# Optimization experiments

Measured on AMD Instinct MI355X. Metric: run time of the kernel, lower is better.

The kernel has to match this reference:

```python
import jax, jax.numpy as jnp
import numpy as np

K = 4                                   # children per internal node (complete K-ary tree)
L = 7                                   # number of tree levels
N = (K**L - 1) // (K - 1)               # 5461 nodes, BFS order, root = node 0
IN_DIM = 512
MEM_DIM = 512
_STARTS = [(K**l - 1) // (K - 1) for l in range(L + 1)]  # node-index range of each level


def _make_children():
    ch = np.full((N, K), -1, dtype=np.int32)
    for n in range(N):
        base = n * K + 1
        if base + K <= N:                # internal node; leaves keep -1 padding
            ch[n] = np.arange(base, base + K, dtype=np.int32)
    return jnp.asarray(ch)


def setup_inputs() -> dict:
    key = jax.random.key(0)
    ks = jax.random.split(key, 40)
    it = iter(range(1, 40))

    def lin(fin, fout):
        s = 1.0 / np.sqrt(fin)           # torch nn.Linear default init
        W = jax.random.uniform(ks[next(it)], (fin, fout), jnp.float32, -s, s)
        b = jax.random.uniform(ks[next(it)], (fout,), jnp.float32, -s, s)
        return W, b

    inp = {
        "x": jax.random.normal(ks[0], (N, IN_DIM), jnp.float32),
        "children": _make_children(),
    }
    for mod in ("vis", "lang"):
        inp[f"W_ioux_{mod}"], inp[f"b_ioux_{mod}"] = lin(IN_DIM, 3 * MEM_DIM)
        inp[f"W_iouh_{mod}"], inp[f"b_iouh_{mod}"] = lin(MEM_DIM, 3 * MEM_DIM)
        inp[f"W_fx_{mod}"], inp[f"b_fx_{mod}"] = lin(IN_DIM, MEM_DIM)
        inp[f"W_fh_{mod}"], inp[f"b_fh_{mod}"] = lin(MEM_DIM, MEM_DIM)
    inp["W_type"], inp["b_type"] = lin(IN_DIM, 2)
    return inp


def _gates(iou_x, fx_n, W_iouh, b_iouh, W_fh, b_fh, child_c, child_h, h_sum):
    # iou_x: [n,3m] precomputed ioux(x); fx_n: [n,m]; child_*: [n,K,m]; h_sum: [n,m]
    iou = iou_x + h_sum @ W_iouh + b_iouh
    i, o, u = jnp.split(iou, 3, axis=-1)
    f = jax.nn.sigmoid(child_h @ W_fh + b_fh + fx_n[:, None, :])   # [n,K,m]
    c = jax.nn.sigmoid(i) * jnp.tanh(u) + (f * child_c).sum(axis=1)
    h = jax.nn.sigmoid(o) * jnp.tanh(c)
    return c, h


def reference(x, children,
              W_ioux_vis, b_ioux_vis, W_iouh_vis, b_iouh_vis,
              W_fx_vis, b_fx_vis, W_fh_vis, b_fh_vis,
              W_ioux_lang, b_ioux_lang, W_iouh_lang, b_iouh_lang,
              W_fx_lang, b_fx_lang, W_fh_lang, b_fh_lang,
              W_type, b_type):
    dt = x.dtype
    # input-side projections for every node at once (batched GEMMs)
    ioux_v = x @ W_ioux_vis + b_ioux_vis
    fx_v = x @ W_fx_vis + b_fx_vis
    ioux_l = x @ W_ioux_lang + b_ioux_lang
    fx_l = x @ W_fx_lang + b_fx_lang
    # eval-mode greedy type selection: one-hot argmax of type_query logits
    sel_lang = jnp.argmax(x @ W_type + b_type, axis=-1) == 0       # [N] True -> lang branch

    c_all = jnp.zeros((N, MEM_DIM), dt)
    h_all = jnp.zeros((N, MEM_DIM), dt)

    for l in range(L - 1, -1, -1):       # bottom-up over tree levels (static loop)
        s, e = _STARTS[l], _STARTS[l + 1]
        ch = children[s:e]               # [n,K]
        m = (ch >= 0)[..., None].astype(dt)
        idx = jnp.where(ch >= 0, ch, 0)
        child_c = c_all[idx] * m         # leaves: all-zero child states (matches original)
        child_h = h_all[idx] * m
        h_sum = child_h.sum(axis=1)
        c_v, h_v = _gates(ioux_v[s:e], fx_v[s:e], W_iouh_vis, b_iouh_vis,
                          W_fh_vis, b_fh_vis, child_c, child_h, h_sum)
        c_l, h_l = _gates(ioux_l[s:e], fx_l[s:e], W_iouh_lang, b_iouh_lang,
                          W_fh_lang, b_fh_lang, child_c, child_h, h_sum)
        lang = sel_lang[s:e][:, None]
        c_all = c_all.at[s:e].set(jnp.where(lang, c_l, c_v))
        h_all = h_all.at[s:e].set(jnp.where(lang, h_l, h_v))
    return h_all                         # up-state h of every node; root at row 0
```

## Files before the change

### kernel.cpp

```cpp
#include <hip/hip_runtime.h>
#include <cstdint>

constexpr int N_NODES = 5461;
constexpr int N_INTERIOR = 1365;

using f16x8 = __attribute__((ext_vector_type(8))) _Float16;
using f32x4 = __attribute__((ext_vector_type(4))) float;

typedef const __attribute__((address_space(1))) unsigned int* gas_p;
typedef __attribute__((address_space(3))) unsigned int* las_p;

__device__ __forceinline__ float sigm(float v) { return 1.0f / (1.0f + __expf(-v)); }

__constant__ int d_STARTS[8] = {0, 1, 5, 21, 85, 341, 1365, 5461};

struct GP {
    const _Float16* Ah[2]; const _Float16* Al[2];
    const _Float16* BhL[2]; const _Float16* BlL[2];
    const _Float16* BhV[2]; const _Float16* BlV[2];
    const float* biasL[2]; const float* biasV[2];
    float* Y[2];
    const int* permA[2];
    const int* cntPtr;
    int cntScale[2];
    int M[2]; int Nout[2]; int yT0;
};

__global__ __launch_bounds__(512, 4)
void gemm_pair(GP g)
{
    const int set = (blockIdx.y < (unsigned)g.yT0) ? 0 : 1;
    const int bn = (set ? (blockIdx.y - g.yT0) : blockIdx.y) * 128;
    const int M = g.M[set];
    const int Nout = g.Nout[set];
    const int nL = g.cntPtr[0] * g.cntScale[set];
    const int nTl = (nL + 127) >> 7;
    const int t = blockIdx.x;
    int rowBase, rowEnd;
    const _Float16 *Bh, *Bl;
    const float* bias;
    if (t < nTl) {
        rowBase = t << 7; rowEnd = nL;
        Bh = g.BhL[set]; Bl = g.BlL[set]; bias = g.biasL[set];
    } else {
        rowBase = nL + ((t - nTl) << 7); rowEnd = M;
        Bh = g.BhV[set]; Bl = g.BlV[set]; bias = g.biasV[set];
    }
    if (rowBase >= rowEnd) return;

    __shared__ _Float16 AsH[2][128 * 32];
    __shared__ _Float16 AsL[2][128 * 32];
    __shared__ _Float16 BsH[2][128 * 32];
    __shared__ _Float16 BsL[2][128 * 32];

    const int tid = threadIdx.x;
    const int wid = tid >> 6;
    const int lane = tid & 63;
    const int wm = (wid >> 2) * 64;
    const int wn = (wid & 3) * 32;
    const int lrow = lane >> 2;
    const int kofs = (lane & 3) * 8;

    int u0 = rowBase + wid * 16 + lrow; if (u0 > rowEnd - 1) u0 = rowEnd - 1;
    const int* permA = g.permA[set];
    const int a0 = permA ? permA[u0] : u0;
    const _Float16* gAh = g.Ah[set] + (size_t)a0 * 512 + kofs;
    const _Float16* gAl = g.Al[set] + (size_t)a0 * 512 + kofs;
    const _Float16* gBh = Bh + (size_t)(bn + wid * 16 + lrow) * 512 + kofs;
    const _Float16* gBl = Bl + (size_t)(bn + wid * 16 + lrow) * 512 + kofs;

    f32x4 acc0[4][2] = {};
    f32x4 acc1[4][2] = {};

    auto stage = [&](int k0, int b) {
        __builtin_amdgcn_global_load_lds((gas_p)(const void*)(gAh + k0), (las_p)(void*)(&AsH[b][wid * 512]), 16, 0, 0);
        __builtin_amdgcn_global_load_lds((gas_p)(const void*)(gAl + k0), (las_p)(void*)(&AsL[b][wid * 512]), 16, 0, 0);
        __builtin_amdgcn_global_load_lds((gas_p)(const void*)(gBh + k0), (las_p)(void*)(&BsH[b][wid * 512]), 16, 0, 0);
        __builtin_amdgcn_global_load_lds((gas_p)(const void*)(gBl + k0), (las_p)(void*)(&BsL[b][wid * 512]), 16, 0, 0);
    };

    const int rsel = lane & 15;
    const int kg = lane >> 4;

    stage(0, 0);
    __syncthreads();
#pragma unroll 1
    for (int step = 0; step < 16; ++step) {
        const int cur = step & 1;
        if (step < 15) stage((step + 1) * 32, cur ^ 1);
        const f16x8* AH = (const f16x8*)AsH[cur];
        const f16x8* AL = (const f16x8*)AsL[cur];
        const f16x8* BH = (const f16x8*)BsH[cur];
        const f16x8* BL = (const f16x8*)BsL[cur];
        f16x8 bh[2], bl[2];
#pragma unroll
        for (int j = 0; j < 2; ++j) {
            bh[j] = BH[(wn + j * 16 + rsel) * 4 + kg];
            bl[j] = BL[(wn + j * 16 + rsel) * 4 + kg];
        }
#pragma unroll
        for (int i = 0; i < 4; ++i) {
            f16x8 ah = AH[(wm + i * 16 + rsel) * 4 + kg];
            f16x8 al = AL[(wm + i * 16 + rsel) * 4 + kg];
#pragma unroll
            for (int j = 0; j < 2; ++j) {
                acc0[i][j] = __builtin_amdgcn_mfma_f32_16x16x32_f16(ah, bh[j], acc0[i][j], 0, 0, 0);
                acc1[i][j] = __builtin_amdgcn_mfma_f32_16x16x32_f16(ah, bl[j], acc1[i][j], 0, 0, 0);
                acc1[i][j] = __builtin_amdgcn_mfma_f32_16x16x32_f16(al, bh[j], acc1[i][j], 0, 0, 0);
            }
        }
        __syncthreads();
    }

    float* Y = g.Y[set];
#pragma unroll
    for (int i = 0; i < 4; ++i) {
        int row0 = rowBase + wm + i * 16 + kg * 4;
#pragma unroll
        for (int j = 0; j < 2; ++j) {
            int col = bn + wn + j * 16 + rsel;
            float bb = bias[col];
#pragma unroll
            for (int r = 0; r < 4; ++r) {
                int row = row0 + r;
                if (row < rowEnd)
                    Y[(size_t)row * Nout + col] = acc0[i][j][r] + acc1[i][j][r] * (1.0f / 2048.0f) + bb;
            }
        }
    }
}

__global__ __launch_bounds__(256)
void cast_x_sel(const float* __restrict__ x, const float* __restrict__ Wt,
                const float* __restrict__ bt,
                _Float16* __restrict__ hi, _Float16* __restrict__ lo,
                int* __restrict__ sel)
{
    __shared__ float s0[256], s1[256];
    int t = threadIdx.x;
    int row = blockIdx.x * 2 + (t >> 7);
    int c0 = (t & 127) * 4;
    float p0 = 0.f, p1 = 0.f;
    if (row < N_NODES) {
        size_t off = (size_t)row * 512 + c0;
        float4 v = *(const float4*)(x + off);
        float vv[4] = {v.x, v.y, v.z, v.w};
        union { _Float16 h[4]; ushort4 u; } H, L;
#pragma unroll
        for (int i = 0; i < 4; ++i) {
            _Float16 h = (_Float16)vv[i];
            H.h[i] = h;
            L.h[i] = (_Float16)((vv[i] - (float)h) * 2048.0f);
            p0 = fmaf(vv[i], Wt[(c0 + i) * 2], p0);
            p1 = fmaf(vv[i], Wt[(c0 + i) * 2 + 1], p1);
        }
        *(ushort4*)(hi + off) = H.u;
        *(ushort4*)(lo + off) = L.u;
    }
    s0[t] = p0; s1[t] = p1;
    __syncthreads();
    for (int st = 64; st > 0; st >>= 1) {
        if ((t & 127) < st) { s0[t] += s0[t + st]; s1[t] += s1[t + st]; }
        __syncthreads();
    }
    if ((t & 127) == 0 && row < N_NODES)
        sel[row] = (s0[t] + bt[0] >= s1[t] + bt[1]) ? 1 : 0;
}

struct WtArgs {
    const float* src[8];
    _Float16* dsth[8];
    _Float16* dstl[8];
    int nout[8];
};

__global__ __launch_bounds__(256)
void transpose_cast(WtArgs a)
{
    int mi = blockIdx.z;
    int Nout = a.nout[mi];
    int n0 = blockIdx.y * 64;
    if (n0 >= Nout) return;
    int k0 = blockIdx.x * 64;
    const float* W = a.src[mi];
    _Float16* TH = a.dsth[mi];
    _Float16* TL = a.dstl[mi];
    __shared__ float t[64][65];
    int tx = threadIdx.x & 63, ty = threadIdx.x >> 6;
#pragma unroll
    for (int r = ty; r < 64; r += 4)
        t[r][tx] = W[(size_t)(k0 + r) * Nout + n0 + tx];
    __syncthreads();
#pragma unroll
    for (int r = ty; r < 64; r += 4) {
        float v = t[tx][r];
        _Float16 h = (_Float16)v;
        TH[(size_t)(n0 + r) * 512 + k0 + tx] = h;
        TL[(size_t)(n0 + r) * 512 + k0 + tx] = (_Float16)((v - (float)h) * 2048.0f);
    }
}

__global__ __launch_bounds__(256)
void partition_kernel(const int* __restrict__ sel, int* __restrict__ perm_g,
                      int* __restrict__ inv_g, int* __restrict__ lvlPerm,
                      int* __restrict__ lvlInv, int* __restrict__ cnt)
{
    __shared__ int ps[256];
    int b = blockIdx.x;
    int s, e;
    if (b == 0) { s = 0; e = N_NODES; }
    else { s = d_STARTS[b - 1]; e = d_STARTS[b]; }
    int E = e - s;
    int t = threadIdx.x;
    int chunk = (E + 255) / 256;
    int beg = min(t * chunk, E);
    int end = min(beg + chunk, E);
    int c = 0;
    for (int i = beg; i < end; ++i) c += sel[s + i];
    ps[t] = c;
    __syncthreads();
    for (int off = 1; off < 256; off <<= 1) {
        int other = (t >= off) ? ps[t - off] : 0;
        __syncthreads();
        ps[t] += other;
        __syncthreads();
    }
    int total = ps[255];
    int excl = ps[t] - c;
    int pL = excl;
    int pV = total + (beg - excl);
    for (int i = beg; i < end; ++i) {
        int node = s + i;
        int pos = sel[node] ? pL++ : pV++;
        int slot = s + pos;
        if (b == 0) { perm_g[slot] = node; inv_g[node] = slot; }
        else { lvlPerm[slot] = node; lvlInv[node] = slot; }
    }
    if (t == 0) cnt[b] = total;
}

__global__ __launch_bounds__(256)
void leaf_gather(const float* __restrict__ iou_pre,
                 const float* __restrict__ b_iouh_v, const float* __restrict__ b_iouh_l,
                 const int* __restrict__ children,
                 const int* __restrict__ lvlPerm, const int* __restrict__ inv_g,
                 const int* __restrict__ cnt,
                 float* __restrict__ c_all, float* __restrict__ h_all,
                 _Float16* __restrict__ hs_h, _Float16* __restrict__ hs_l,
                 _Float16* __restrict__ ch_h, _Float16* __restrict__ ch_l)
{
    int ip = blockIdx.x;
    int p = lvlPerm[341 + ip];
    int t = threadIdx.x;
    int d0 = t * 2;
    int nLg = cnt[0];
    float hsum[2] = {0.f, 0.f};
#pragma unroll
    for (int k = 0; k < 4; ++k) {
        int cnode = children[p * 4 + k];
        int u = inv_g[cnode];
        const float* bh = (u < nLg) ? b_iouh_l : b_iouh_v;
        size_t ub = (size_t)u * 1536;
#pragma unroll
        for (int e = 0; e < 2; ++e) {
            int d = d0 + e;
            float iv = iou_pre[ub + d]        + bh[d];
            float ov = iou_pre[ub + 512 + d]  + bh[512 + d];
            float uv = iou_pre[ub + 1024 + d] + bh[1024 + d];
            float cc = sigm(iv) * tanhf(uv);
            float hh = sigm(ov) * tanhf(cc);
            c_all[(size_t)cnode * 512 + d] = cc;
            h_all[(size_t)cnode * 512 + d] = hh;
            hsum[e] += hh;
            _Float16 hf = (_Float16)hh;
            size_t o = ((size_t)(ip * 4 + k)) * 512 + d;
            ch_h[o] = hf;
            ch_l[o] = (_Float16)((hh - (float)hf) * 2048.0f);
        }
    }
#pragma unroll
    for (int e = 0; e < 2; ++e) {
        _Float16 sh = (_Float16)hsum[e];
        hs_h[(size_t)ip * 512 + d0 + e] = sh;
        hs_l[(size_t)ip * 512 + d0 + e] = (_Float16)((hsum[e] - (float)sh) * 2048.0f);
    }
}

__global__ __launch_bounds__(256)
void combine_gather(int sPar, int sLvl,
    const float* __restrict__ iou_pre, const float* __restrict__ fx_pre,
    const float* __restrict__ iou_h, const float* __restrict__ fpre,
    const int* __restrict__ lvlPerm, const int* __restrict__ lvlInv,
    const int* __restrict__ inv_g, const int* __restrict__ children,
    float* __restrict__ c_all, float* __restrict__ h_all,
    _Float16* __restrict__ hs_h, _Float16* __restrict__ hs_l,
    _Float16* __restrict__ ch_h, _Float16* __restrict__ ch_l)
{
    int ip = blockIdx.x;
    int p = lvlPerm[sPar + ip];
    int t = threadIdx.x;
    int d0 = t * 2;
    float hsum[2] = {0.f, 0.f};
#pragma unroll
    for (int k = 0; k < 4; ++k) {
        int cnode = children[p * 4 + k];
        int j = lvlInv[cnode] - sLvl;
        int u = inv_g[cnode];
        size_t ub = (size_t)u * 1536;
        size_t jb = (size_t)j * 1536;
#pragma unroll
        for (int e = 0; e < 2; ++e) {
            int d = d0 + e;
            float iv = iou_pre[ub + d]        + iou_h[jb + d];
            float ov = iou_pre[ub + 512 + d]  + iou_h[jb + 512 + d];
            float uv = iou_pre[ub + 1024 + d] + iou_h[jb + 1024 + d];
            float fxn = fx_pre[(size_t)u * 512 + d];
            float csum = 0.f;
#pragma unroll
            for (int k2 = 0; k2 < 4; ++k2) {
                int gc = children[cnode * 4 + k2];
                float f = sigm(fpre[((size_t)(j * 4 + k2)) * 512 + d] + fxn);
                csum = fmaf(f, c_all[(size_t)gc * 512 + d], csum);
            }
            float cc = sigm(iv) * tanhf(uv) + csum;
            float hh = sigm(ov) * tanhf(cc);
            c_all[(size_t)cnode * 512 + d] = cc;
            h_all[(size_t)cnode * 512 + d] = hh;
            hsum[e] += hh;
            _Float16 hf = (_Float16)hh;
            size_t o = ((size_t)(ip * 4 + k)) * 512 + d;
            ch_h[o] = hf;
            ch_l[o] = (_Float16)((hh - (float)hf) * 2048.0f);
        }
    }
#pragma unroll
    for (int e = 0; e < 2; ++e) {
        _Float16 sh = (_Float16)hsum[e];
        hs_h[(size_t)ip * 512 + d0 + e] = sh;
        hs_l[(size_t)ip * 512 + d0 + e] = (_Float16)((hsum[e] - (float)sh) * 2048.0f);
    }
}

__global__ __launch_bounds__(256)
void combine_root(
    const float* __restrict__ iou_pre, const float* __restrict__ fx_pre,
    const float* __restrict__ iou_h, const float* __restrict__ fpre,
    const int* __restrict__ inv_g, const int* __restrict__ children,
    float* __restrict__ c_all, float* __restrict__ h_all)
{
    int d = blockIdx.x * 256 + threadIdx.x;
    if (d >= 512) return;
    int u = inv_g[0];
    size_t ub = (size_t)u * 1536;
    float iv = iou_pre[ub + d]        + iou_h[d];
    float ov = iou_pre[ub + 512 + d]  + iou_h[512 + d];
    float uv = iou_pre[ub + 1024 + d] + iou_h[1024 + d];
    float fxn = fx_pre[(size_t)u * 512 + d];
    float csum = 0.f;
#pragma unroll
    for (int k = 0; k < 4; ++k) {
        int gc = children[k];
        float f = sigm(fpre[(size_t)k * 512 + d] + fxn);
        csum = fmaf(f, c_all[(size_t)gc * 512 + d], csum);
    }
    float cc = sigm(iv) * tanhf(uv) + csum;
    float hh = sigm(ov) * tanhf(cc);
    c_all[d] = cc;
    h_all[d] = hh;
}

extern "C" void kernel_launch(void* const* d_in, const int* in_sizes, int n_in,
                              void* d_out, int out_size, void* d_ws, size_t ws_size,
                              hipStream_t stream)
{
    const float* x        = (const float*)d_in[0];
    const int*   children = (const int*)  d_in[1];
    const float* W_ioux_v = (const float*)d_in[2];
    const float* b_ioux_v = (const float*)d_in[3];
    const float* W_iouh_v = (const float*)d_in[4];
    const float* b_iouh_v = (const float*)d_in[5];
    const float* W_fx_v   = (const float*)d_in[6];
    const float* b_fx_v   = (const float*)d_in[7];
    const float* W_fh_v   = (const float*)d_in[8];
    const float* b_fh_v   = (const float*)d_in[9];
    const float* W_ioux_l = (const float*)d_in[10];
    const float* b_ioux_l = (const float*)d_in[11];
    const float* W_iouh_l = (const float*)d_in[12];
    const float* b_iouh_l = (const float*)d_in[13];
    const float* W_fx_l   = (const float*)d_in[14];
    const float* b_fx_l   = (const float*)d_in[15];
    const float* W_fh_l   = (const float*)d_in[16];
    const float* b_fh_l   = (const float*)d_in[17];
    const float* W_type   = (const float*)d_in[18];
    const float* b_type   = (const float*)d_in[19];
    float* h_all = (float*)d_out;

    float* p = (float*)d_ws;
    float* iou_pre = p; p += (size_t)N_NODES * 1536;
    float* fx_pre  = p; p += (size_t)N_NODES * 512;
    float* c_all   = p; p += (size_t)N_NODES * 512;
    float* iou_h   = p; p += (size_t)1024 * 1536;
    float* fpre    = p; p += (size_t)4096 * 512;
    int* sel     = (int*)p; p += 6144;
    int* perm_g  = (int*)p; p += 6144;
    int* inv_g   = (int*)p; p += 6144;
    int* lvlPerm = (int*)p; p += 2048;
    int* lvlInv  = (int*)p; p += 2048;
    int* cnt     = (int*)p; p += 64;
    _Float16* q = (_Float16*)p;
    _Float16* xh   = q; q += (size_t)N_NODES * 512;
    _Float16* xl   = q; q += (size_t)N_NODES * 512;
    _Float16* hs_h = q; q += (size_t)1024 * 512;
    _Float16* hs_l = q; q += (size_t)1024 * 512;
    _Float16* ch_h = q; q += (size_t)4096 * 512;
    _Float16* ch_l = q; q += (size_t)4096 * 512;
    _Float16* wt_ioux_vh = q; q += (size_t)1536 * 512;
    _Float16* wt_ioux_vl = q; q += (size_t)1536 * 512;
    _Float16* wt_ioux_lh = q; q += (size_t)1536 * 512;
    _Float16* wt_ioux_ll = q; q += (size_t)1536 * 512;
    _Float16* wt_iouh_vh = q; q += (size_t)1536 * 512;
    _Float16* wt_iouh_vl = q; q += (size_t)1536 * 512;
    _Float16* wt_iouh_lh = q; q += (size_t)1536 * 512;
    _Float16* wt_iouh_ll = q; q += (size_t)1536 * 512;
    _Float16* wt_fx_vh   = q; q += (size_t)512 * 512;
    _Float16* wt_fx_vl   = q; q += (size_t)512 * 512;
    _Float16* wt_fx_lh   = q; q += (size_t)512 * 512;
    _Float16* wt_fx_ll   = q; q += (size_t)512 * 512;
    _Float16* wt_fh_vh   = q; q += (size_t)512 * 512;
    _Float16* wt_fh_vl   = q; q += (size_t)512 * 512;
    _Float16* wt_fh_lh   = q; q += (size_t)512 * 512;
    _Float16* wt_fh_ll   = q; q += (size_t)512 * 512;

    cast_x_sel<<<(N_NODES + 1) / 2, 256, 0, stream>>>(x, W_type, b_type, xh, xl, sel);

    WtArgs wa;
    wa.src[0] = W_ioux_v; wa.dsth[0] = wt_ioux_vh; wa.dstl[0] = wt_ioux_vl; wa.nout[0] = 1536;
    wa.src[1] = W_ioux_l; wa.dsth[1] = wt_ioux_lh; wa.dstl[1] = wt_ioux_ll; wa.nout[1] = 1536;
    wa.src[2] = W_iouh_v; wa.dsth[2] = wt_iouh_vh; wa.dstl[2] = wt_iouh_vl; wa.nout[2] = 1536;
    wa.src[3] = W_iouh_l; wa.dsth[3] = wt_iouh_lh; wa.dstl[3] = wt_iouh_ll; wa.nout[3] = 1536;
    wa.src[4] = W_fx_v;   wa.dsth[4] = wt_fx_vh;   wa.dstl[4] = wt_fx_vl;   wa.nout[4] = 512;
    wa.src[5] = W_fx_l;   wa.dsth[5] = wt_fx_lh;   wa.dstl[5] = wt_fx_ll;   wa.nout[5] = 512;
    wa.src[6] = W_fh_v;   wa.dsth[6] = wt_fh_vh;   wa.dstl[6] = wt_fh_vl;   wa.nout[6] = 512;
    wa.src[7] = W_fh_l;   wa.dsth[7] = wt_fh_lh;   wa.dstl[7] = wt_fh_ll;   wa.nout[7] = 512;
    transpose_cast<<<dim3(8, 24, 8), 256, 0, stream>>>(wa);

    partition_kernel<<<7, 256, 0, stream>>>(sel, perm_g, inv_g, lvlPerm, lvlInv, cnt);

    {
        GP g{};
        g.Ah[0] = xh; g.Al[0] = xl;       g.Ah[1] = xh; g.Al[1] = xl;
        g.BhL[0] = wt_ioux_lh; g.BlL[0] = wt_ioux_ll; g.BhV[0] = wt_ioux_vh; g.BlV[0] = wt_ioux_vl;
        g.BhL[1] = wt_fx_lh;   g.BlL[1] = wt_fx_ll;   g.BhV[1] = wt_fx_vh;   g.BlV[1] = wt_fx_vl;
        g.biasL[0] = b_ioux_l; g.biasV[0] = b_ioux_v;
        g.biasL[1] = b_fx_l;   g.biasV[1] = b_fx_v;
        g.Y[0] = iou_pre; g.Y[1] = fx_pre;
        g.permA[0] = perm_g; g.permA[1] = perm_g;
        g.cntPtr = cnt; g.cntScale[0] = 1; g.cntScale[1] = 1;
        g.M[0] = N_NODES; g.M[1] = N_NODES;
        g.Nout[0] = 1536; g.Nout[1] = 512;
        g.yT0 = 12;
        gemm_pair<<<dim3(44, 16), 512, 0, stream>>>(g);
    }

    leaf_gather<<<1024, 256, 0, stream>>>(iou_pre, b_iouh_v, b_iouh_l, children,
        lvlPerm, inv_g, cnt, c_all, h_all, hs_h, hs_l, ch_h, ch_l);

    static const int STARTS[8] = {0, 1, 5, 21, 85, 341, 1365, 5461};
    for (int l = 5; l >= 0; --l) {
        int s = STARTS[l];
        int E = STARTS[l + 1] - s;
        GP g{};
        g.Ah[0] = hs_h; g.Al[0] = hs_l;   g.Ah[1] = ch_h; g.Al[1] = ch_l;
        g.BhL[0] = wt_iouh_lh; g.BlL[0] = wt_iouh_ll; g.BhV[0] = wt_iouh_vh; g.BlV[0] = wt_iouh_vl;
        g.BhL[1] = wt_fh_lh;   g.BlL[1] = wt_fh_ll;   g.BhV[1] = wt_fh_vh;   g.BlV[1] = wt_fh_vl;
        g.biasL[0] = b_iouh_l; g.biasV[0] = b_iouh_v;
        g.biasL[1] = b_fh_l;   g.biasV[1] = b_fh_v;
        g.Y[0] = iou_h; g.Y[1] = fpre;
        g.permA[0] = nullptr; g.permA[1] = nullptr;
        g.cntPtr = cnt + 1 + l; g.cntScale[0] = 1; g.cntScale[1] = 4;
        g.M[0] = E; g.M[1] = E * 4;
        g.Nout[0] = 1536; g.Nout[1] = 512;
        g.yT0 = 12;
        int gx = 1 + (E * 4 + 127) / 128;
        gemm_pair<<<dim3(gx, 16), 512, 0, stream>>>(g);
        if (l > 0) {
            int sPar = STARTS[l - 1];
            int nPar = s - sPar;
            combine_gather<<<nPar, 256, 0, stream>>>(sPar, s,
                iou_pre, fx_pre, iou_h, fpre, lvlPerm, lvlInv, inv_g, children,
                c_all, h_all, hs_h, hs_l, ch_h, ch_l);
        } else {
            combine_root<<<2, 256, 0, stream>>>(iou_pre, fx_pre, iou_h, fpre,
                inv_g, children, c_all, h_all);
        }
    }
}
```

Measured before the change: 262.3 us.

## Use 4-wave GEMM blocks with 64x64 warp tiles and XOR-swizzled LDS

The gemm_pair kernel now runs with 256 threads (4 waves) instead of 512. Each wave computes a 64x64 output tile instead of 64x32, and each thread stages two rows per operand per k-step. The LDS layout gains an XOR swizzle on the 16-byte chunk index, applied both to the global source offset and to the read index, to reduce bank conflicts on the MFMA operand reads. This doubles register reuse of the A and B fragments per wave, but raises accumulator register pressure and halves the waves per block, so there is less latency hiding.

Result: slower. 295.5 us (+12.6%).

```diff
diff --git a/kernel.cpp b/kernel.cpp
--- a/kernel.cpp
+++ b/kernel.cpp
@@ -26,13 +26,12 @@
     int M[2]; int Nout[2]; int yT0;
 };
 
-__global__ __launch_bounds__(512, 4)
+__global__ __launch_bounds__(256, 2)
 void gemm_pair(GP g)
 {
     const int set = (blockIdx.y < (unsigned)g.yT0) ? 0 : 1;
     const int bn = (set ? (blockIdx.y - g.yT0) : blockIdx.y) * 128;
     const int M = g.M[set];
-    const int Nout = g.Nout[set];
     const int nL = g.cntPtr[0] * g.cntScale[set];
     const int nTl = (nL + 127) >> 7;
     const int t = blockIdx.x;
@@ -56,31 +55,45 @@
     const int tid = threadIdx.x;
     const int wid = tid >> 6;
     const int lane = tid & 63;
-    const int wm = (wid >> 2) * 64;
-    const int wn = (wid & 3) * 32;
-    const int lrow = lane >> 2;
-    const int kofs = (lane & 3) * 8;
-
-    int u0 = rowBase + wid * 16 + lrow; if (u0 > rowEnd - 1) u0 = rowEnd - 1;
-    const int* permA = g.permA[set];
-    const int a0 = permA ? permA[u0] : u0;
-    const _Float16* gAh = g.Ah[set] + (size_t)a0 * 512 + kofs;
-    const _Float16* gAl = g.Al[set] + (size_t)a0 * 512 + kofs;
-    const _Float16* gBh = Bh + (size_t)(bn + wid * 16 + lrow) * 512 + kofs;
-    const _Float16* gBl = Bl + (size_t)(bn + wid * 16 + lrow) * 512 + kofs;
-
-    f32x4 acc0[4][2] = {};
-    f32x4 acc1[4][2] = {};
-
-    auto stage = [&](int k0, int b) {
-        __builtin_amdgcn_global_load_lds((gas_p)(const void*)(gAh + k0), (las_p)(void*)(&AsH[b][wid * 512]), 16, 0, 0);
-        __builtin_amdgcn_global_load_lds((gas_p)(const void*)(gAl + k0), (las_p)(void*)(&AsL[b][wid * 512]), 16, 0, 0);
-        __builtin_amdgcn_global_load_lds((gas_p)(const void*)(gBh + k0), (las_p)(void*)(&BsH[b][wid * 512]), 16, 0, 0);
-        __builtin_amdgcn_global_load_lds((gas_p)(const void*)(gBl + k0), (las_p)(void*)(&BsL[b][wid * 512]), 16, 0, 0);
-    };
-
+    const int wm = (wid >> 1) * 64;
+    const int wn = (wid & 1) * 64;
     const int rsel = lane & 15;
     const int kg = lane >> 4;
+
+    const int srow0 = wid * 32 + (lane >> 2);
+    const int srow1 = srow0 + 16;
+    const int csrc = (((lane & 3) ^ ((lane >> 3) & 3))) * 8;
+    const int* permA = g.permA[set];
+    int aR0 = rowBase + srow0; if (aR0 > rowEnd - 1) aR0 = rowEnd - 1;
+    int aR1 = rowBase + srow1; if (aR1 > rowEnd - 1) aR1 = rowEnd - 1;
+    const int a0 = permA ? permA[aR0] : aR0;
+    const int a1 = permA ? permA[aR1] : aR1;
+    const _Float16* pAh0 = g.Ah[set] + (size_t)a0 * 512 + csrc;
+    const _Float16* pAl0 = g.Al[set] + (size_t)a0 * 512 + csrc;
+    const _Float16* pAh1 = g.Ah[set] + (size_t)a1 * 512 + csrc;
+    const _Float16* pAl1 = g.Al[set] + (size_t)a1 * 512 + csrc;
+    const _Float16* pBh0 = Bh + (size_t)(bn + srow0) * 512 + csrc;
+    const _Float16* pBl0 = Bl + (size_t)(bn + srow0) * 512 + csrc;
+    const _Float16* pBh1 = Bh + (size_t)(bn + srow1) * 512 + csrc;
+    const _Float16* pBl1 = Bl + (size_t)(bn + srow1) * 512 + csrc;
+    const int ldsOfs0 = wid * 1024;
+    const int ldsOfs1 = wid * 1024 + 512;
+
+    f32x4 acc0[4][4] = {};
+    f32x4 acc1[4][4] = {};
+
+    auto stage = [&](int k0, int b) {
+        __builtin_amdgcn_global_load_lds((gas_p)(const void*)(pAh0 + k0), (las_p)(void*)(&AsH[b][ldsOfs0]), 16, 0, 0);
+        __builtin_amdgcn_global_load_lds((gas_p)(const void*)(pAh1 + k0), (las_p)(void*)(&AsH[b][ldsOfs1]), 16, 0, 0);
+        __builtin_amdgcn_global_load_lds((gas_p)(const void*)(pAl0 + k0), (las_p)(void*)(&AsL[b][ldsOfs0]), 16, 0, 0);
+        __builtin_amdgcn_global_load_lds((gas_p)(const void*)(pAl1 + k0), (las_p)(void*)(&AsL[b][ldsOfs1]), 16, 0, 0);
+        __builtin_amdgcn_global_load_lds((gas_p)(const void*)(pBh0 + k0), (las_p)(void*)(&BsH[b][ldsOfs0]), 16, 0, 0);
+        __builtin_amdgcn_global_load_lds((gas_p)(const void*)(pBh1 + k0), (las_p)(void*)(&BsH[b][ldsOfs1]), 16, 0, 0);
+        __builtin_amdgcn_global_load_lds((gas_p)(const void*)(pBl0 + k0), (las_p)(void*)(&BsL[b][ldsOfs0]), 16, 0, 0);
+        __builtin_amdgcn_global_load_lds((gas_p)(const void*)(pBl1 + k0), (las_p)(void*)(&BsL[b][ldsOfs1]), 16, 0, 0);
+    };
+
+    const int sl = kg ^ ((rsel >> 1) & 3);
 
     stage(0, 0);
     __syncthreads();
@@ -92,18 +105,20 @@
         const f16x8* AL = (const f16x8*)AsL[cur];
         const f16x8* BH = (const f16x8*)BsH[cur];
         const f16x8* BL = (const f16x8*)BsL[cur];
-        f16x8 bh[2], bl[2];
-#pragma unroll
-        for (int j = 0; j < 2; ++j) {
-            bh[j] = BH[(wn + j * 16 + rsel) * 4 + kg];
-            bl[j] = BL[(wn + j * 16 + rsel) * 4 + kg];
+        f16x8 bh[4], bl[4];
+#pragma unroll
+        for (int j = 0; j < 4; ++j) {
+            int bi = (wn + j * 16 + rsel) * 4 + sl;
+            bh[j] = BH[bi];
+            bl[j] = BL[bi];
         }
 #pragma unroll
         for (int i = 0; i < 4; ++i) {
-            f16x8 ah = AH[(wm + i * 16 + rsel) * 4 + kg];
-            f16x8 al = AL[(wm + i * 16 + rsel) * 4 + kg];
-#pragma unroll
-            for (int j = 0; j < 2; ++j) {
+            int ai = (wm + i * 16 + rsel) * 4 + sl;
+            f16x8 ah = AH[ai];
+            f16x8 al = AL[ai];
+#pragma unroll
+            for (int j = 0; j < 4; ++j) {
                 acc0[i][j] = __builtin_amdgcn_mfma_f32_16x16x32_f16(ah, bh[j], acc0[i][j], 0, 0, 0);
                 acc1[i][j] = __builtin_amdgcn_mfma_f32_16x16x32_f16(ah, bl[j], acc1[i][j], 0, 0, 0);
                 acc1[i][j] = __builtin_amdgcn_mfma_f32_16x16x32_f16(al, bh[j], acc1[i][j], 0, 0, 0);
@@ -113,11 +128,12 @@
     }
 
     float* Y = g.Y[set];
+    const int Nout = g.Nout[set];
 #pragma unroll
     for (int i = 0; i < 4; ++i) {
         int row0 = rowBase + wm + i * 16 + kg * 4;
 #pragma unroll
-        for (int j = 0; j < 2; ++j) {
+        for (int j = 0; j < 4; ++j) {
             int col = bn + wn + j * 16 + rsel;
             float bb = bias[col];
 #pragma unroll
@@ -459,7 +475,7 @@
         g.M[0] = N_NODES; g.M[1] = N_NODES;
         g.Nout[0] = 1536; g.Nout[1] = 512;
         g.yT0 = 12;
-        gemm_pair<<<dim3(44, 16), 512, 0, stream>>>(g);
+        gemm_pair<<<dim3(44, 16), 256, 0, stream>>>(g);
     }
 
     leaf_gather<<<1024, 256, 0, stream>>>(iou_pre, b_iouh_v, b_iouh_l, children,
@@ -482,7 +498,7 @@
         g.Nout[0] = 1536; g.Nout[1] = 512;
         g.yT0 = 12;
         int gx = 1 + (E * 4 + 127) / 128;
-        gemm_pair<<<dim3(gx, 16), 512, 0, stream>>>(g);
+        gemm_pair<<<dim3(gx, 16), 256, 0, stream>>>(g);
         if (l > 0) {
             int sPar = STARTS[l - 1];
             int nPar = s - sPar;
```
